# Optimization experiments

Measured on AMD Instinct MI355X. Metric: run time of the kernel, lower is better.

## Reference

```python
import jax, jax.numpy as jnp
import numpy as np

B, N, H, NH = 2, 48, 256, 8
DH = H // NH  # attention head size = 32


def setup_inputs() -> dict:
    key = jax.random.key(0)
    ks = jax.random.split(key, 12)
    s = 0.02
    return {
        "attention_mask": jnp.zeros((B, 1, N, N), jnp.float32),
        "structure_matrix_pair": jax.random.normal(ks[0], (B, N, N, H), jnp.float32),
        "structure_matrix_triplet": jax.random.normal(ks[1], (B, N, N, N, H), jnp.float32),
        # Linear weights stored [in, out] (x @ W + b == torch Linear with W.T)
        "Wq": jax.random.normal(ks[2], (H, H), jnp.float32) * s, "bq": jnp.zeros((H,), jnp.float32),
        "Wk": jax.random.normal(ks[3], (H, H), jnp.float32) * s, "bk": jnp.zeros((H,), jnp.float32),
        "Wv": jax.random.normal(ks[4], (H, H), jnp.float32) * s, "bv": jnp.zeros((H,), jnp.float32),
        "Wsq": jax.random.normal(ks[5], (H, DH), jnp.float32) * s, "bsq": jnp.zeros((DH,), jnp.float32),
        "Wsk": jax.random.normal(ks[6], (H, DH), jnp.float32) * s, "bsk": jnp.zeros((DH,), jnp.float32),
        "Wsv": jax.random.normal(ks[7], (H, DH), jnp.float32) * s, "bsv": jnp.zeros((DH,), jnp.float32),
    }


def reference(attention_mask, structure_matrix_pair, structure_matrix_triplet,
              Wq, bq, Wk, bk, Wv, bv, Wsq, bsq, Wsk, bsk, Wsv, bsv):
    def heads(x):  # [B,N,N,H] -> [B,NH,N,N,DH]
        return x.reshape(B, N, N, NH, DH).transpose(0, 3, 1, 2, 4)

    q = heads(structure_matrix_pair @ Wq + bq)[:, :, :, None, :, :]  # [B,h,N,1,N,dh]
    k = heads(structure_matrix_pair @ Wk + bk)[:, :, :, :, None, :]  # [B,h,N,N,1,dh]
    v = heads(structure_matrix_pair @ Wv + bv)[:, :, :, None, :, :]  # [B,h,N,1,N,dh]

    sq = (structure_matrix_triplet @ Wsq + bsq)[:, None]  # [B,1,N,N,N,dh]
    sk = (structure_matrix_triplet @ Wsk + bsk)[:, None]
    sv = (structure_matrix_triplet @ Wsv + bsv)[:, None]

    q = q + sq  # [B,h,N,N,N,dh]
    k = k + sk
    v = v + sv

    scores = jnp.sum(q * k, axis=-1) / np.sqrt(DH).astype(np.float32)  # [B,h,N,N,N]
    scores = scores + attention_mask[:, :, None, :, :]
    probs = jax.nn.softmax(scores, axis=-1)
    # dropout is identity in eval mode
    ctx = jnp.einsum('bhikj,bhikjd->bhikd', probs, v)  # sum over last N (j)
    # [B,h,N,N,dh] -> [B,N,N,h*dh]
    return ctx.transpose(0, 2, 3, 1, 4).reshape(B, N, N, NH * DH)
```

## Files before the change

kernel.cpp:

```cpp
#include <hip/hip_runtime.h>
#include <hip/hip_bf16.h>

#define B_ 2
#define N_ 48
#define H_ 256
#define NH_ 8
#define DH_ 32
#define SQS_LD 100

typedef __attribute__((ext_vector_type(8))) short bf16x8;
typedef __attribute__((ext_vector_type(4))) float f32x4;

__device__ __forceinline__ unsigned short f2bf(float f) {
  unsigned u = __float_as_uint(f);
  u += 0x7FFFu + ((u >> 16) & 1u);
  return (unsigned short)(u >> 16);
}

__device__ __forceinline__ bf16x8 cvt8(float4 x, float4 y) {
  union { unsigned u[4]; bf16x8 v; } o;
  asm("v_cvt_pk_bf16_f32 %0, %1, %2" : "=v"(o.u[0]) : "v"(x.x), "v"(x.y));
  asm("v_cvt_pk_bf16_f32 %0, %1, %2" : "=v"(o.u[1]) : "v"(x.z), "v"(x.w));
  asm("v_cvt_pk_bf16_f32 %0, %1, %2" : "=v"(o.u[2]) : "v"(y.x), "v"(y.y));
  asm("v_cvt_pk_bf16_f32 %0, %1, %2" : "=v"(o.u[3]) : "v"(y.z), "v"(y.w));
  return o.v;
}

__global__ void pack_kernel(const float* __restrict__ Wq, const float* __restrict__ Wk,
                            const float* __restrict__ Wv, const float* __restrict__ bq,
                            const float* __restrict__ bk, const float* __restrict__ bv,
                            const float* __restrict__ Wsq, const float* __restrict__ Wsk,
                            const float* __restrict__ Wsv, const float* __restrict__ bsq,
                            const float* __restrict__ bsk, const float* __restrict__ bsv,
                            unsigned short* __restrict__ wfrag_pair,
                            unsigned short* __restrict__ wfrag_main,
                            float* __restrict__ biascat, float* __restrict__ biasm) {
  int t = blockIdx.x * 256 + threadIdx.x;
  if (t < 196608) {
    int i8 = t & 7, lane = (t >> 3) & 63, kt = (t >> 9) & 7, nt = t >> 12;
    int k = kt * 32 + ((lane >> 4) << 3) + i8;
    int n = nt * 16 + (lane & 15);
    const float* W = (n < 256) ? Wq : (n < 512) ? Wk : Wv;
    wfrag_pair[t] = f2bf(W[k * 256 + (n & 255)]);
  } else if (t < 196608 + 24576) {
    int p = t - 196608;
    int i8 = p & 7, lane = (p >> 3) & 63, kt = (p >> 9) & 7, nt = p >> 12;
    int k = kt * 32 + ((lane >> 4) << 3) + i8;
    int n = nt * 16 + (lane & 15);
    const float* W = (n < 32) ? Wsq : (n < 64) ? Wsk : Wsv;
    wfrag_main[p] = f2bf(W[k * 32 + (n & 31)]);
  } else if (t < 196608 + 24576 + 768) {
    int p = t - 196608 - 24576;
    const float* bsrc = (p < 256) ? bq : (p < 512) ? bk : bv;
    biascat[p] = bsrc[p & 255];
  } else if (t < 196608 + 24576 + 768 + 96) {
    int p = t - 196608 - 24576 - 768;
    biasm[p] = (p < 32) ? bsq[p] : (p < 64) ? bsk[p - 32] : bsv[p - 64];
  }
}

__device__ __forceinline__ void stage48x256(const float* __restrict__ src, char* tAc, int tid) {
#pragma unroll
  for (int it = 0; it < 4; ++it) {
    int c = it * 384 + tid;
    const float4* g = reinterpret_cast<const float4*>(src) + (c << 1);
    float4 x = g[0];
    float4 y = g[1];
    int row = c >> 5;
    int off = (row << 9) + ((c & 31) << 4);
    off ^= (row & 7) << 4;
    *reinterpret_cast<bf16x8*>(tAc + off) = cvt8(x, y);
  }
}

__global__ __launch_bounds__(384, 3)
void pair_proj_kernel(const float* __restrict__ pair,
                      const unsigned short* __restrict__ wfrag_pair,
                      const float* __restrict__ biascat, float* __restrict__ proj) {
  __shared__ __align__(16) char tAc[48 * 256 * 2];
  int tid = threadIdx.x;
  int lane = tid & 63;
  int wave = tid >> 6;
  int gm = blockIdx.x >> 3;
  int gn = blockIdx.x & 7;

  stage48x256(pair + (size_t)gm * 12288, tAc, tid);

  bf16x8 wf[8];
  {
    const bf16x8* wp = reinterpret_cast<const bf16x8*>(wfrag_pair);
#pragma unroll
    for (int kt = 0; kt < 8; ++kt) wf[kt] = wp[((gn * 6 + wave) * 8 + kt) * 64 + lane];
  }
  __syncthreads();

  f32x4 acc[3];
#pragma unroll
  for (int mt = 0; mt < 3; ++mt) acc[mt] = (f32x4){0.f, 0.f, 0.f, 0.f};
#pragma unroll
  for (int kt = 0; kt < 8; ++kt) {
#pragma unroll
    for (int mt = 0; mt < 3; ++mt) {
      int row = mt * 16 + (lane & 15);
      int off = (row << 9) + (kt << 6) + ((lane >> 4) << 4);
      off ^= (row & 7) << 4;
      bf16x8 a = *reinterpret_cast<const bf16x8*>(tAc + off);
      acc[mt] = __builtin_amdgcn_mfma_f32_16x16x32_bf16(a, wf[kt], acc[mt], 0, 0, 0);
    }
  }

  int col = gn * 96 + wave * 16 + (lane & 15);
  float bias = biascat[col];
  int jb = (lane >> 4) * 4;
#pragma unroll
  for (int mt = 0; mt < 3; ++mt) {
#pragma unroll
    for (int rr = 0; rr < 4; ++rr) {
      int j = mt * 16 + jb + rr;
      proj[(size_t)(gm * 48 + j) * 768 + col] = acc[mt][rr] + bias;
    }
  }
}

__global__ __launch_bounds__(384, 6)
void e2e_fused(const float* __restrict__ mask, const float* __restrict__ trip,
               const float* __restrict__ proj, const unsigned short* __restrict__ wfragm,
               const float* __restrict__ biasm, float* __restrict__ out) {
  __shared__ __align__(16) char smem[48 * 256 * 2];
  __shared__ float khl[256];
  __shared__ float pbuf[8][48];
  char* tAc = smem;
  float* sqS = reinterpret_cast<float*>(smem);

  int tid = threadIdx.x;
  int lane = tid & 63;
  int wave = tid >> 6;

  int bid = blockIdx.x;
  int s = (bid & 7) * 576 + (bid >> 3);
  int g = s / 48;
  int k = s % 48;
  int b = g / 48;
  int rowbase = g * 48;

  stage48x256(trip + (size_t)s * 12288, tAc, tid);
  if (tid < 256) khl[tid] = proj[(size_t)s * 768 + 256 + tid];
  __syncthreads();

  const bf16x8* wp = reinterpret_cast<const bf16x8*>(wfragm);
  f32x4 acc[3];
#pragma unroll
  for (int mt = 0; mt < 3; ++mt) acc[mt] = (f32x4){0.f, 0.f, 0.f, 0.f};
#pragma unroll
  for (int kt = 0; kt < 8; ++kt) {
    bf16x8 w = wp[(wave * 8 + kt) * 64 + lane];
#pragma unroll
    for (int mt = 0; mt < 3; ++mt) {
      int row = mt * 16 + (lane & 15);
      int off = (row << 9) + (kt << 6) + ((lane >> 4) << 4);
      off ^= (row & 7) << 4;
      bf16x8 a = *reinterpret_cast<const bf16x8*>(tAc + off);
      acc[mt] = __builtin_amdgcn_mfma_f32_16x16x32_bf16(a, w, acc[mt], 0, 0, 0);
    }
  }
  __syncthreads();

  {
    int n = wave * 16 + (lane & 15);
    float bias = biasm[n];
    int jb = (lane >> 4) * 4;
#pragma unroll
    for (int mt = 0; mt < 3; ++mt) {
#pragma unroll
      for (int rr = 0; rr < 4; ++rr)
        sqS[(mt * 16 + jb + rr) * SQS_LD + n] = acc[mt][rr] + bias;
    }
  }
  __syncthreads();

  {
    int j = tid % 48, h = tid / 48;
    const float4* q4 = reinterpret_cast<const float4*>(proj + (size_t)(rowbase + j) * 768 + h * 32);
    const float4* sq4 = reinterpret_cast<const float4*>(sqS + j * SQS_LD);
    const float4* kh4 = reinterpret_cast<const float4*>(khl + h * 32);
    float sc = 0.f;
#pragma unroll
    for (int d4 = 0; d4 < 8; ++d4) {
      float4 q = q4[d4];
      float4 sq = sq4[d4];
      float4 sk = sq4[8 + d4];
      float4 kh = kh4[d4];
      sc += (q.x + sq.x) * (kh.x + sk.x);
      sc += (q.y + sq.y) * (kh.y + sk.y);
      sc += (q.z + sq.z) * (kh.z + sk.z);
      sc += (q.w + sq.w) * (kh.w + sk.w);
    }
    pbuf[h][j] = sc * 0.17677669529663687f + mask[b * 2304 + k * 48 + j];
  }
  __syncthreads();

  for (int h = wave; h < 8; h += 6) {
    float x = (lane < 48) ? pbuf[h][lane] : -INFINITY;
    float m = x;
#pragma unroll
    for (int off = 32; off; off >>= 1) m = fmaxf(m, __shfl_xor(m, off));
    float e = (lane < 48) ? __expf(x - m) : 0.f;
    float sum = e;
#pragma unroll
    for (int off = 32; off; off >>= 1) sum += __shfl_xor(sum, off);
    if (lane < 48) pbuf[h][lane] = e / sum;
  }
  __syncthreads();

  if (tid < 256) {
    int h = tid >> 5, d = tid & 31;
    const float* vbase = proj + (size_t)rowbase * 768 + 512 + tid;
    float a = 0.f;
#pragma unroll 8
    for (int j = 0; j < 48; ++j)
      a += pbuf[h][j] * (vbase[(size_t)j * 768] + sqS[j * SQS_LD + 64 + d]);
    out[(size_t)s * 256 + tid] = a;
  }
}

extern "C" void kernel_launch(void* const* d_in, const int* in_sizes, int n_in,
                              void* d_out, int out_size, void* d_ws, size_t ws_size,
                              hipStream_t stream) {
  const float* mask = (const float*)d_in[0];
  const float* pair = (const float*)d_in[1];
  const float* trip = (const float*)d_in[2];
  const float* Wq = (const float*)d_in[3];
  const float* bq = (const float*)d_in[4];
  const float* Wk = (const float*)d_in[5];
  const float* bk = (const float*)d_in[6];
  const float* Wv = (const float*)d_in[7];
  const float* bv = (const float*)d_in[8];
  const float* Wsq = (const float*)d_in[9];
  const float* bsq = (const float*)d_in[10];
  const float* Wsk = (const float*)d_in[11];
  const float* bsk = (const float*)d_in[12];
  const float* Wsv = (const float*)d_in[13];
  const float* bsv = (const float*)d_in[14];

  char* ws = (char*)d_ws;
  float* proj = (float*)ws;
  unsigned short* wfrag_pair = (unsigned short*)(ws + 14155776);
  unsigned short* wfrag_main = (unsigned short*)(ws + 14155776 + 393216);
  float* biascat = (float*)(ws + 14155776 + 393216 + 49152);
  float* biasm = (float*)(ws + 14155776 + 393216 + 49152 + 3072);

  pack_kernel<<<867, 256, 0, stream>>>(Wq, Wk, Wv, bq, bk, bv, Wsq, Wsk, Wsv,
                                       bsq, bsk, bsv,
                                       wfrag_pair, wfrag_main, biascat, biasm);
  pair_proj_kernel<<<768, 384, 0, stream>>>(pair, wfrag_pair, biascat, proj);
  e2e_fused<<<4608, 384, 0, stream>>>(mask, trip, proj, wfrag_main, biasm,
                                      (float*)d_out);
}
```

Before: 84.15 us.

## Split PV into bf16 MFMA for sv term and rebalance score computation

Only three waves now run the triplet projection GEMM, each holding two output tiles with the weight fragments prefetched one step ahead. The sv projection is written transposed as bf16 into shared memory, and the probability-times-sv sum is done with a small MFMA over bf16 probabilities. The shared-memory sq/sk stride shrinks to 68 floats. Scores are computed by 8-lane groups per row with shuffle reductions instead of one thread per (h,j), and the remaining v-term loop reads probabilities as float4. This adds extra zeroing, syncs and LDS buffers, and rounds probabilities and sv to bf16, which reduces precision in the output.

```diff
diff --git a/kernel.cpp b/kernel.cpp
--- a/kernel.cpp
+++ b/kernel.cpp
@@ -6,7 +6,7 @@
 #define H_ 256
 #define NH_ 8
 #define DH_ 32
-#define SQS_LD 100
+#define SQS_LD 68
 
 typedef __attribute__((ext_vector_type(8))) short bf16x8;
 typedef __attribute__((ext_vector_type(4))) float f32x4;
@@ -127,6 +127,9 @@
                const float* __restrict__ proj, const unsigned short* __restrict__ wfragm,
                const float* __restrict__ biasm, float* __restrict__ out) {
   __shared__ __align__(16) char smem[48 * 256 * 2];
+  __shared__ __align__(16) unsigned short svT[32 * 64];
+  __shared__ __align__(16) unsigned short pA[16 * 64];
+  __shared__ float m2buf[8][32];
   __shared__ float khl[256];
   __shared__ float pbuf[8][48];
   char* tAc = smem;
@@ -145,57 +148,106 @@
 
   stage48x256(trip + (size_t)s * 12288, tAc, tid);
   if (tid < 256) khl[tid] = proj[(size_t)s * 768 + 256 + tid];
-  __syncthreads();
-
-  const bf16x8* wp = reinterpret_cast<const bf16x8*>(wfragm);
-  f32x4 acc[3];
-#pragma unroll
-  for (int mt = 0; mt < 3; ++mt) acc[mt] = (f32x4){0.f, 0.f, 0.f, 0.f};
-#pragma unroll
-  for (int kt = 0; kt < 8; ++kt) {
-    bf16x8 w = wp[(wave * 8 + kt) * 64 + lane];
-#pragma unroll
-    for (int mt = 0; mt < 3; ++mt) {
-      int row = mt * 16 + (lane & 15);
-      int off = (row << 9) + (kt << 6) + ((lane >> 4) << 4);
-      off ^= (row & 7) << 4;
-      bf16x8 a = *reinterpret_cast<const bf16x8*>(tAc + off);
-      acc[mt] = __builtin_amdgcn_mfma_f32_16x16x32_bf16(a, w, acc[mt], 0, 0, 0);
-    }
-  }
-  __syncthreads();
-
   {
-    int n = wave * 16 + (lane & 15);
-    float bias = biasm[n];
+    unsigned* zp = reinterpret_cast<unsigned*>(pA);
+    unsigned* zs = reinterpret_cast<unsigned*>(svT);
+    zp[tid < 384 ? tid : tid] = 0;
+    if (tid < 128) zp[384 + tid] = 0;
+    zs[tid] = 0;
+    zs[384 + tid] = 0;
+    if (tid < 256) zs[768 + tid] = 0;
+  }
+  __syncthreads();
+
+  f32x4 acc[3][2];
+#pragma unroll
+  for (int mt = 0; mt < 3; ++mt)
+#pragma unroll
+    for (int tt = 0; tt < 2; ++tt) acc[mt][tt] = (f32x4){0.f, 0.f, 0.f, 0.f};
+  if (wave < 3) {
+    const bf16x8* wp = reinterpret_cast<const bf16x8*>(wfragm);
+    bf16x8 wc0 = wp[((wave * 2 + 0) * 8 + 0) * 64 + lane];
+    bf16x8 wc1 = wp[((wave * 2 + 1) * 8 + 0) * 64 + lane];
+#pragma unroll
+    for (int kt = 0; kt < 8; ++kt) {
+      bf16x8 wn0, wn1;
+      if (kt < 7) {
+        wn0 = wp[((wave * 2 + 0) * 8 + kt + 1) * 64 + lane];
+        wn1 = wp[((wave * 2 + 1) * 8 + kt + 1) * 64 + lane];
+      }
+#pragma unroll
+      for (int mt = 0; mt < 3; ++mt) {
+        int row = mt * 16 + (lane & 15);
+        int off = (row << 9) + (kt << 6) + ((lane >> 4) << 4);
+        off ^= (row & 7) << 4;
+        bf16x8 a = *reinterpret_cast<const bf16x8*>(tAc + off);
+        acc[mt][0] = __builtin_amdgcn_mfma_f32_16x16x32_bf16(a, wc0, acc[mt][0], 0, 0, 0);
+        acc[mt][1] = __builtin_amdgcn_mfma_f32_16x16x32_bf16(a, wc1, acc[mt][1], 0, 0, 0);
+      }
+      wc0 = wn0;
+      wc1 = wn1;
+    }
+  }
+  __syncthreads();
+
+  if (wave < 2) {
     int jb = (lane >> 4) * 4;
 #pragma unroll
-    for (int mt = 0; mt < 3; ++mt) {
-#pragma unroll
-      for (int rr = 0; rr < 4; ++rr)
-        sqS[(mt * 16 + jb + rr) * SQS_LD + n] = acc[mt][rr] + bias;
+    for (int tt = 0; tt < 2; ++tt) {
+      int n = wave * 32 + tt * 16 + (lane & 15);
+      float bias = biasm[n];
+#pragma unroll
+      for (int mt = 0; mt < 3; ++mt)
+#pragma unroll
+        for (int rr = 0; rr < 4; ++rr)
+          sqS[(mt * 16 + jb + rr) * SQS_LD + n] = acc[mt][tt][rr] + bias;
+    }
+  } else if (wave == 2) {
+    int jb = (lane >> 4) * 4;
+#pragma unroll
+    for (int tt = 0; tt < 2; ++tt) {
+      int d = tt * 16 + (lane & 15);
+      float bias = biasm[64 + d];
+#pragma unroll
+      for (int mt = 0; mt < 3; ++mt)
+#pragma unroll
+        for (int rr = 0; rr < 4; ++rr) {
+          int j = mt * 16 + jb + rr;
+          int off = (d << 7) + (j << 1);
+          off ^= (d & 7) << 4;
+          *reinterpret_cast<unsigned short*>(reinterpret_cast<char*>(svT) + off) =
+              f2bf(acc[mt][tt][rr] + bias);
+        }
     }
   }
   __syncthreads();
 
   {
-    int j = tid % 48, h = tid / 48;
-    const float4* q4 = reinterpret_cast<const float4*>(proj + (size_t)(rowbase + j) * 768 + h * 32);
-    const float4* sq4 = reinterpret_cast<const float4*>(sqS + j * SQS_LD);
-    const float4* kh4 = reinterpret_cast<const float4*>(khl + h * 32);
-    float sc = 0.f;
-#pragma unroll
-    for (int d4 = 0; d4 < 8; ++d4) {
-      float4 q = q4[d4];
-      float4 sq = sq4[d4];
-      float4 sk = sq4[8 + d4];
-      float4 kh = kh4[d4];
-      sc += (q.x + sq.x) * (kh.x + sk.x);
-      sc += (q.y + sq.y) * (kh.y + sk.y);
-      sc += (q.z + sq.z) * (kh.z + sk.z);
-      sc += (q.w + sq.w) * (kh.w + sk.w);
-    }
-    pbuf[h][j] = sc * 0.17677669529663687f + mask[b * 2304 + k * 48 + j];
+    int j = tid >> 3, dq = tid & 7;
+    float4 sq = *reinterpret_cast<const float4*>(sqS + j * SQS_LD + dq * 4);
+    float4 sk = *reinterpret_cast<const float4*>(sqS + j * SQS_LD + 32 + dq * 4);
+    const float* qrow = proj + (size_t)(rowbase + j) * 768;
+    float val[8];
+#pragma unroll
+    for (int h = 0; h < 8; ++h) {
+      float4 q = *reinterpret_cast<const float4*>(qrow + h * 32 + dq * 4);
+      float4 kh = *reinterpret_cast<const float4*>(khl + h * 32 + dq * 4);
+      float v = (q.x + sq.x) * (kh.x + sk.x);
+      v += (q.y + sq.y) * (kh.y + sk.y);
+      v += (q.z + sq.z) * (kh.z + sk.z);
+      v += (q.w + sq.w) * (kh.w + sk.w);
+      val[h] = v;
+    }
+#pragma unroll
+    for (int h = 0; h < 8; ++h) {
+      val[h] += __shfl_xor(val[h], 1);
+      val[h] += __shfl_xor(val[h], 2);
+      val[h] += __shfl_xor(val[h], 4);
+    }
+    float sc = val[0];
+#pragma unroll
+    for (int h = 1; h < 8; ++h) sc = (dq == h) ? val[h] : sc;
+    pbuf[dq][j] = sc * 0.17677669529663687f + mask[b * 2304 + k * 48 + j];
   }
   __syncthreads();
 
@@ -208,19 +260,52 @@
     float sum = e;
 #pragma unroll
     for (int off = 32; off; off >>= 1) sum += __shfl_xor(sum, off);
-    if (lane < 48) pbuf[h][lane] = e / sum;
-  }
-  __syncthreads();
-
+    if (lane < 48) {
+      float p = e / sum;
+      pbuf[h][lane] = p;
+      int off = (h << 7) + (lane << 1);
+      off ^= (h & 7) << 4;
+      *reinterpret_cast<unsigned short*>(reinterpret_cast<char*>(pA) + off) = f2bf(p);
+    }
+  }
+  __syncthreads();
+
+  if (wave < 2) {
+    f32x4 c2 = (f32x4){0.f, 0.f, 0.f, 0.f};
+#pragma unroll
+    for (int ks = 0; ks < 2; ++ks) {
+      int ra = ((lane & 15) << 7) + (ks << 6) + ((lane >> 4) << 4);
+      ra ^= (lane & 7) << 4;
+      bf16x8 pa = *reinterpret_cast<const bf16x8*>(reinterpret_cast<char*>(pA) + ra);
+      int d = (lane & 15) + wave * 16;
+      int rb = (d << 7) + (ks << 6) + ((lane >> 4) << 4);
+      rb ^= (d & 7) << 4;
+      bf16x8 bv = *reinterpret_cast<const bf16x8*>(reinterpret_cast<char*>(svT) + rb);
+      c2 = __builtin_amdgcn_mfma_f32_16x16x32_bf16(pa, bv, c2, 0, 0, 0);
+    }
+    if (lane < 32) {
+      int h0 = (lane >> 4) * 4;
+      int d = (lane & 15) + wave * 16;
+#pragma unroll
+      for (int r = 0; r < 4; ++r) m2buf[h0 + r][d] = c2[r];
+    }
+  }
+
+  float a_ = 0.f;
   if (tid < 256) {
-    int h = tid >> 5, d = tid & 31;
+    int h = tid >> 5;
     const float* vbase = proj + (size_t)rowbase * 768 + 512 + tid;
-    float a = 0.f;
-#pragma unroll 8
-    for (int j = 0; j < 48; ++j)
-      a += pbuf[h][j] * (vbase[(size_t)j * 768] + sqS[j * SQS_LD + 64 + d]);
-    out[(size_t)s * 256 + tid] = a;
-  }
+#pragma unroll 3
+    for (int j4 = 0; j4 < 12; ++j4) {
+      float4 p4 = *reinterpret_cast<const float4*>(&pbuf[h][j4 * 4]);
+      a_ += p4.x * vbase[(j4 * 4 + 0) * 768];
+      a_ += p4.y * vbase[(j4 * 4 + 1) * 768];
+      a_ += p4.z * vbase[(j4 * 4 + 2) * 768];
+      a_ += p4.w * vbase[(j4 * 4 + 3) * 768];
+    }
+  }
+  __syncthreads();
+  if (tid < 256) out[(size_t)s * 256 + tid] = a_ + m2buf[tid >> 5][tid & 31];
 }
 
 extern "C" void kernel_launch(void* const* d_in, const int* in_sizes, int n_in,
```

Result: slower. 87.67 us (+4.2%).
